# Kernel tuning notes

Hardware: AMD Instinct MI355X
Metric: run time of the kernel (lower is better)

The kernel has to match this reference:

```python
import jax, jax.numpy as jnp
import numpy as np

N, DIM, H, HD, RD, QLR, OLR, G = 64, 4096, 32, 192, 64, 1536, 512, 8
BS, MAXB, L, NBLK, TOPK, EPS = 64, 64, 4096, 4096, 1024, 1e-6
SLOTS = NBLK * BS
SCALE = HD ** -0.5
NEG = -1e30


def _rms(x, w, eps=EPS):
    return x * jax.lax.rsqrt(jnp.mean(x * x, -1, keepdims=True) + eps) * w


def _rope(x, pos):
    # x: [..., RD]; pos broadcastable to x.shape[:-1]; interleaved pairs
    half = RD // 2
    inv = 1.0 / (10000.0 ** (jnp.arange(half, dtype=jnp.float32) * 2.0 / RD))
    ang = pos[..., None].astype(jnp.float32) * inv  # [..., half]
    c, s = jnp.cos(ang), jnp.sin(ang)
    xr = x.reshape(x.shape[:-1] + (half, 2))
    x0, x1 = xr[..., 0], xr[..., 1]
    return jnp.stack([x0 * c - x1 * s, x0 * s + x1 * c], -1).reshape(x.shape)


def setup_inputs() -> dict:
    key = jax.random.key(0)
    ks = jax.random.split(key, 12)
    block_tables = jax.random.permutation(ks[0], jnp.arange(N * MAXB, dtype=jnp.int32)).reshape(N, MAXB)
    context_lens = jax.random.randint(ks[1], (N,), 1, L, dtype=jnp.int32)
    last = context_lens - 1
    slot_mapping = (block_tables[jnp.arange(N), last // BS] * BS + last % BS).astype(jnp.int32)
    def w(k, shape, fan_in):
        return jax.random.normal(k, shape, jnp.float32) * (fan_in ** -0.5)
    return {
        'x': jax.random.normal(ks[2], (N, DIM), jnp.float32),
        'kv_cache': jax.random.normal(ks[3], (SLOTS, HD), jnp.float32),
        'block_tables': block_tables,
        'context_lens': context_lens,
        'slot_mapping': slot_mapping,
        'wq_a_w': w(ks[4], (QLR, DIM), DIM),
        'q_norm_w': jnp.ones((QLR,), jnp.float32),
        'wq_b_w': w(ks[5], (H * HD, QLR), QLR),
        'wkv_w': w(ks[6], (HD, DIM), DIM),
        'kv_norm_w': jnp.ones((HD,), jnp.float32),
        'wo_a_w': w(ks[7], (G, OLR, H * HD // G), H * HD // G),
        'wo_b_w': w(ks[8], (DIM, G * OLR), G * OLR),
        'attn_sink': jax.random.normal(ks[9], (H,), jnp.float32),
    }


def reference(x, kv_cache, block_tables, context_lens, slot_mapping,
              wq_a_w, q_norm_w, wq_b_w, wkv_w, kv_norm_w,
              wo_a_w, wo_b_w, attn_sink):
    pos = (context_lens - 1).astype(jnp.float32)  # [N] query positions
    # --- queries: LoRA down-proj -> RMSNorm -> up-proj -> heads ---
    q = _rms(x @ wq_a_w.T, q_norm_w) @ wq_b_w.T            # [N, H*HD]
    q = q.reshape(N, H, HD)
    q = jnp.concatenate([q[..., :HD - RD], _rope(q[..., HD - RD:], pos[:, None])], -1)
    # --- new KV latent + paged write (slot_mapping scatter) ---
    kv = _rms(x @ wkv_w.T, kv_norm_w)                       # [N, HD]
    kv = jnp.concatenate([kv[:, :HD - RD], _rope(kv[:, HD - RD:], pos)], -1)
    cache = kv_cache.at[slot_mapping].set(kv)
    # --- paged gather into dense per-request view [N, L, HD] ---
    ar = jnp.arange(L)
    slot = block_tables[:, ar // BS] * BS + ar % BS         # [N, L]
    valid = ar[None, :] < context_lens[:, None]             # [N, L]
    kv_dense = cache[jnp.where(valid, slot, 0)]
    kv_dense = jnp.where(valid[..., None], kv_dense, 0.0)
    # --- sparse top-k attention with sink logit ---
    logits = jnp.einsum('nhd,nld->nhl', q, kv_dense) * SCALE
    logits = jnp.where(valid[:, None, :], logits, NEG)
    vals, idx = jax.lax.top_k(logits, TOPK)                 # [N, H, K]
    sink = attn_sink[None, :, None]                         # [1, H, 1]
    m = jnp.maximum(jnp.max(vals, -1, keepdims=True), sink)
    e = jnp.exp(vals - m)
    denom = jnp.sum(e, -1, keepdims=True) + jnp.exp(sink - m)
    p = e / denom                                           # [N, H, K]
    probs = jnp.put_along_axis(jnp.zeros_like(logits), idx, p, axis=-1, inplace=False)
    o = jnp.einsum('nhl,nld->nhd', probs, kv_dense)         # [N, H, HD]
    # --- grouped LoRA output projection ---
    og = o.reshape(N, G, H * HD // G)
    lat = jnp.einsum('ngi,goi->ngo', og, wo_a_w).reshape(N, G * OLR)
    return lat @ wo_b_w.T                                   # [N, DIM]
```

## Files before the change

kernel.cpp:

```cpp
#include <hip/hip_runtime.h>
#include <hip/hip_bf16.h>

static constexpr float EPS_   = 1e-6f;
static constexpr float SCALE_ = 0.07216878364870323f;
static constexpr float LOG2_1E4_OVER_32 = 13.287712379549449f / 32.0f;

static constexpr long OFF_QLAT = 0;
static constexpr long OFF_Q    = OFF_QLAT + 64L * 1536;
static constexpr long OFF_KVR  = OFF_Q    + 64L * 6144;
static constexpr long OFF_O    = OFF_KVR  + 64L * 192;
static constexpr long OFF_LAT  = OFF_O    + 64L * 6144;
static constexpr long ZERO_F   = OFF_LAT  + 64L * 4096;
static constexpr long OFF_SELM = ZERO_F;
static constexpr long OFF_SELI = OFF_SELM + 2048;
static constexpr long OFF_SELT = OFF_SELI + 2048;
static constexpr long OFF_LOG  = OFF_SELT + 2048;

typedef __attribute__((ext_vector_type(8))) short bf16x8;
typedef __attribute__((ext_vector_type(4))) float f32x4;

__device__ __forceinline__ unsigned fkey(float f) {
    unsigned u = __float_as_uint(f);
    return (u & 0x80000000u) ? ~u : (u | 0x80000000u);
}
__device__ __forceinline__ float kval(unsigned k) {
    unsigned u = (k & 0x80000000u) ? (k ^ 0x80000000u) : ~k;
    return __uint_as_float(u);
}
__device__ __forceinline__ unsigned short f2bf(float f) {
    __hip_bfloat16 h = __float2bfloat16(f);
    return *reinterpret_cast<unsigned short*>(&h);
}
__device__ __forceinline__ bf16x8 pack8(float4 v0, float4 v1) {
    bf16x8 s;
    s[0] = (short)f2bf(v0.x); s[1] = (short)f2bf(v0.y);
    s[2] = (short)f2bf(v0.z); s[3] = (short)f2bf(v0.w);
    s[4] = (short)f2bf(v1.x); s[5] = (short)f2bf(v1.y);
    s[6] = (short)f2bf(v1.z); s[7] = (short)f2bf(v1.w);
    return s;
}

__device__ __forceinline__ void hist_add_agg(int* hist, unsigned bin, bool pred) {
    const int lane = (int)(threadIdx.x & 63);
    while (__any(pred)) {
        unsigned long long act = __ballot(pred);
        int leader = __ffsll((unsigned long long)act) - 1;
        unsigned lbin = (unsigned)__shfl((int)bin, leader, 64);
        bool mine = pred && (bin == lbin);
        unsigned long long grp = __ballot(mine);
        if (lane == leader) atomicAdd(&hist[lbin], (int)__popcll(grp));
        if (mine) pred = false;
    }
}

template <int TN>
__global__ __launch_bounds__(256) void gemm_mfma(
    const float* __restrict__ Xb, const float* __restrict__ Wb,
    float* __restrict__ Cb, int K, int ldX, int ldC, int kslice,
    long sXz, long sWz, long sCz)
{
    const float* X = Xb + (long)blockIdx.z * sXz;
    const float* W = Wb + (long)blockIdx.z * sWz;
    float*       C = Cb + (long)blockIdx.z * sCz;
    const int col0 = blockIdx.x * TN;
    const int k0   = blockIdx.y * kslice;

    __shared__ unsigned short Xs[64 * 64];
    __shared__ unsigned short Ws[TN * 64];

    const int t = threadIdx.x;
    const int w = t >> 6, lane = t & 63;
    const int m16 = lane & 15, qd = lane >> 4;
    constexpr int NT = TN / 64;

    f32x4 acc[4][NT];
#pragma unroll
    for (int mt = 0; mt < 4; ++mt)
#pragma unroll
        for (int nt = 0; nt < NT; ++nt) acc[mt][nt] = (f32x4){0.f, 0.f, 0.f, 0.f};

    for (int kt = k0; kt < k0 + kslice; kt += 64) {
#pragma unroll
        for (int i = 0; i < 2; ++i) {
            int idx = t + i * 256;
            int r = idx >> 3, u = idx & 7;
            const float* p = X + (long)r * ldX + kt + u * 8;
            float4 v0 = *(const float4*)p, v1 = *(const float4*)(p + 4);
            *(bf16x8*)(Xs + r * 64 + (u ^ (r & 7)) * 8) = pack8(v0, v1);
        }
#pragma unroll
        for (int i = 0; i < TN / 32; ++i) {
            int idx = t + i * 256;
            int r = idx >> 3, u = idx & 7;
            const float* p = W + (long)(col0 + r) * K + kt + u * 8;
            float4 v0 = *(const float4*)p, v1 = *(const float4*)(p + 4);
            *(bf16x8*)(Ws + r * 64 + (u ^ (r & 7)) * 8) = pack8(v0, v1);
        }
        __syncthreads();
#pragma unroll
        for (int ks = 0; ks < 2; ++ks) {
            int u = ks * 4 + qd;
            bf16x8 a[4], b[NT];
#pragma unroll
            for (int mt = 0; mt < 4; ++mt) {
                int row = mt * 16 + m16;
                a[mt] = *(const bf16x8*)(Xs + row * 64 + (u ^ (row & 7)) * 8);
            }
#pragma unroll
            for (int nt = 0; nt < NT; ++nt) {
                int row = (w * NT + nt) * 16 + m16;
                b[nt] = *(const bf16x8*)(Ws + row * 64 + (u ^ (row & 7)) * 8);
            }
#pragma unroll
            for (int mt = 0; mt < 4; ++mt)
#pragma unroll
                for (int nt = 0; nt < NT; ++nt)
                    acc[mt][nt] = __builtin_amdgcn_mfma_f32_16x16x32_bf16(a[mt], b[nt], acc[mt][nt], 0, 0, 0);
        }
        __syncthreads();
    }
#pragma unroll
    for (int mt = 0; mt < 4; ++mt)
#pragma unroll
        for (int nt = 0; nt < NT; ++nt) {
            int col = col0 + (w * NT + nt) * 16 + m16;
#pragma unroll
            for (int r = 0; r < 4; ++r) {
                int row = mt * 16 + qd * 4 + r;
                atomicAdd(&C[(long)row * ldC + col], acc[mt][nt][r]);
            }
        }
}

__global__ __launch_bounds__(256) void rms_rows(
    float* __restrict__ x, const float* __restrict__ w, int len)
{
    __shared__ float fred[4];
    float* row = x + (long)blockIdx.x * len;
    int t = threadIdx.x;
    float ss = 0.f;
    for (int l = t; l < len; l += 256) { float v = row[l]; ss += v * v; }
#pragma unroll
    for (int off = 32; off; off >>= 1) ss += __shfl_xor(ss, off, 64);
    if ((t & 63) == 0) fred[t >> 6] = ss;
    __syncthreads();
    ss = fred[0] + fred[1] + fred[2] + fred[3];
    float scale = rsqrtf(ss / (float)len + EPS_);
    for (int l = t; l < len; l += 256) row[l] = row[l] * scale * w[l];
}

__global__ __launch_bounds__(256) void rope_q(float* __restrict__ q,
                                              const int* __restrict__ cl)
{
    int n = blockIdx.x;
    float pos = (float)(cl[n] - 1);
    int t = threadIdx.x;
#pragma unroll
    for (int i = 0; i < 4; ++i) {
        int f = t + i * 256;
        int h = f >> 5, r = f & 31;
        float inv = exp2f(-(float)r * LOG2_1E4_OVER_32);
        float ang = pos * inv;
        float sn, cs;
        sincosf(ang, &sn, &cs);
        float* p = q + (long)n * 6144 + h * 192 + 128 + 2 * r;
        float x0 = p[0], x1 = p[1];
        p[0] = x0 * cs - x1 * sn;
        p[1] = x0 * sn + x1 * cs;
    }
}

__global__ __launch_bounds__(256) void kv_post(
    const float* __restrict__ kvr, const float* __restrict__ wnorm,
    const int* __restrict__ cl, const int* __restrict__ smap,
    float* __restrict__ kvcache)
{
    __shared__ float s[192];
    __shared__ float fred[4];
    int n = blockIdx.x, t = threadIdx.x;
    float v = (t < 192) ? kvr[(long)n * 192 + t] : 0.f;
    float ss = v * v;
#pragma unroll
    for (int off = 32; off; off >>= 1) ss += __shfl_xor(ss, off, 64);
    if ((t & 63) == 0) fred[t >> 6] = ss;
    __syncthreads();
    ss = fred[0] + fred[1] + fred[2] + fred[3];
    float scale = rsqrtf(ss / 192.f + EPS_);
    if (t < 192) s[t] = v * scale * wnorm[t];
    __syncthreads();
    if (t < 32) {
        float pos = (float)(cl[n] - 1);
        float inv = exp2f(-(float)t * LOG2_1E4_OVER_32);
        float ang = pos * inv;
        float sn, cs;
        sincosf(ang, &sn, &cs);
        float x0 = s[128 + 2 * t], x1 = s[128 + 2 * t + 1];
        s[128 + 2 * t]     = x0 * cs - x1 * sn;
        s[128 + 2 * t + 1] = x0 * sn + x1 * cs;
    }
    __syncthreads();
    if (t < 192) kvcache[(long)smap[n] * 192 + t] = s[t];
}

__global__ __launch_bounds__(256) void attn_logits_mfma(
    const float* __restrict__ q, const float* __restrict__ kvc,
    const int* __restrict__ bt, const int* __restrict__ cl,
    float* __restrict__ logits)
{
    const int n = blockIdx.y, sbase = blockIdx.x * 256;
    const int ctx = cl[n];
    if (sbase >= ctx) return;

    __shared__ unsigned short qs[32 * 192];
    __shared__ unsigned short kvs[128 * 192];
    const int t = threadIdx.x;
    const int w = t >> 6, lane = t & 63;
    const int m16 = lane & 15, qd = lane >> 4;

#pragma unroll
    for (int i = 0; i < 3; ++i) {
        int idx = t + i * 256;
        int h = idx / 24, u = idx - h * 24;
        const float* p = q + (long)n * 6144 + h * 192 + u * 8;
        float4 v0 = *(const float4*)p, v1 = *(const float4*)(p + 4);
        *(bf16x8*)(qs + h * 192 + (u ^ (h & 7)) * 8) = pack8(v0, v1);
    }

    for (int c = 0; c < 2; ++c) {
        const int base = sbase + c * 128;
        if (base >= ctx) break;

#pragma unroll
        for (int i = 0; i < 12; ++i) {
            int idx = t + i * 256;
            int l = idx / 24, u = idx - l * 24;
            int gl = min(base + l, ctx - 1);
            int slot = bt[n * 64 + (gl >> 6)] * 64 + (gl & 63);
            const float* p = kvc + (long)slot * 192 + u * 8;
            float4 v0 = *(const float4*)p, v1 = *(const float4*)(p + 4);
            *(bf16x8*)(kvs + l * 192 + (u ^ (l & 7)) * 8) = pack8(v0, v1);
        }
        __syncthreads();

        f32x4 acc[2][2];
#pragma unroll
        for (int mt = 0; mt < 2; ++mt)
#pragma unroll
            for (int nt = 0; nt < 2; ++nt) acc[mt][nt] = (f32x4){0.f, 0.f, 0.f, 0.f};

#pragma unroll
        for (int ks = 0; ks < 6; ++ks) {
            int u = ks * 4 + qd;
            bf16x8 a[2], b[2];
#pragma unroll
            for (int mt = 0; mt < 2; ++mt) {
                int row = mt * 16 + m16;
                a[mt] = *(const bf16x8*)(qs + row * 192 + (u ^ (row & 7)) * 8);
            }
#pragma unroll
            for (int nt = 0; nt < 2; ++nt) {
                int row = (2 * w + nt) * 16 + m16;
                b[nt] = *(const bf16x8*)(kvs + row * 192 + (u ^ (row & 7)) * 8);
            }
#pragma unroll
            for (int mt = 0; mt < 2; ++mt)
#pragma unroll
                for (int nt = 0; nt < 2; ++nt)
                    acc[mt][nt] = __builtin_amdgcn_mfma_f32_16x16x32_bf16(a[mt], b[nt], acc[mt][nt], 0, 0, 0);
        }
#pragma unroll
        for (int mt = 0; mt < 2; ++mt)
#pragma unroll
            for (int nt = 0; nt < 2; ++nt) {
                int l = base + (2 * w + nt) * 16 + m16;
#pragma unroll
                for (int r = 0; r < 4; ++r) {
                    int h = mt * 16 + qd * 4 + r;
                    logits[((long)(n * 32 + h) << 12) + l] = acc[mt][nt][r] * SCALE_;
                }
            }
        __syncthreads();
    }
}

__global__ __launch_bounds__(256) void select_topk(
    const float* __restrict__ logits, const int* __restrict__ cl,
    const float* __restrict__ sink, float* __restrict__ selm,
    float* __restrict__ seli, unsigned* __restrict__ selt)
{
    int nh = blockIdx.x, n = nh >> 5, h = nh & 31;
    int ctx = cl[n];
    const float* row = logits + ((long)nh << 12);

    __shared__ unsigned keys[4096];
    __shared__ int hist[256];
    __shared__ float fred[4];
    __shared__ int wsumi[4];
    __shared__ unsigned s_pref;
    __shared__ int s_R;

    int t = threadIdx.x;
    int lane = t & 63, wv = t >> 6;
    bool need_radix = (ctx > 1024);

    hist[t] = 0;
    __syncthreads();

    float mx = -3.0e38f;
    for (int l0 = 0; l0 < ctx; l0 += 256) {
        int l = l0 + t;
        bool valid = l < ctx;
        unsigned k = 0;
        if (valid) {
            float v = row[l];
            k = fkey(v);
            keys[l] = k;
            mx = fmaxf(mx, v);
        }
        if (need_radix) hist_add_agg(hist, k >> 24, valid);
    }
#pragma unroll
    for (int off = 32; off; off >>= 1) mx = fmaxf(mx, __shfl_xor(mx, off, 64));
    if (lane == 0) fred[wv] = mx;
    __syncthreads();
    mx = fmaxf(fmaxf(fred[0], fred[1]), fmaxf(fred[2], fred[3]));

    unsigned tau = 0;
    if (need_radix) {
        unsigned pref = 0;
        int R = 1024;
        for (int round = 3; round >= 0; --round) {
            int sh = round * 8;
            if (round < 3) {
                hist[t] = 0;
                __syncthreads();
                for (int l0 = 0; l0 < ctx; l0 += 256) {
                    int l = l0 + t;
                    if (l < ctx) {
                        unsigned k = keys[l];
                        if ((k >> (sh + 8)) == (pref >> (sh + 8)))
                            atomicAdd(&hist[(k >> sh) & 255], 1);
                    }
                }
                __syncthreads();
            }
            int hv = hist[t];
            int v = hv;
#pragma unroll
            for (int off = 1; off < 64; off <<= 1) {
                int u2 = __shfl_down(v, off, 64);
                if (lane + off < 64) v += u2;
            }
            if (lane == 0) wsumi[wv] = v;
            __syncthreads();
            int above = 0;
#pragma unroll
            for (int w2 = 1; w2 < 4; ++w2)
                if (wv + w2 < 4) above += wsumi[wv + w2];
            int cum = (v - hv) + above;
            if (cum < R && cum + hv >= R) {
                s_pref = pref | ((unsigned)t << sh);
                s_R = R - cum;
            }
            __syncthreads();
            pref = s_pref;
            R = s_R;
            __syncthreads();
        }
        tau = pref;
    }

    float m = fmaxf(mx, sink[h]);
    float part = 0.f;
    for (int l = t; l < ctx; l += 256) {
        unsigned k = keys[l];
        if (k >= tau) part += __expf(kval(k) - m);
    }
#pragma unroll
    for (int off = 32; off; off >>= 1) part += __shfl_xor(part, off, 64);
    __syncthreads();
    if (lane == 0) fred[wv] = part;
    __syncthreads();
    if (t == 0) {
        float denom = fred[0] + fred[1] + fred[2] + fred[3] + __expf(sink[h] - m);
        selm[nh] = m;
        seli[nh] = 1.0f / denom;
        selt[nh] = tau;
    }
}

__global__ __launch_bounds__(256) void attn_wsum_mfma(
    const float* __restrict__ logits, const float* __restrict__ kvc,
    const int* __restrict__ bt, const int* __restrict__ cl,
    const float* __restrict__ selm, const float* __restrict__ seli,
    const unsigned* __restrict__ selt, float* __restrict__ o)
{
    const int n = blockIdx.y, sbase = blockIdx.x * 256;
    const int ctx = cl[n];
    if (sbase >= ctx) return;

    __shared__ unsigned short ps[32 * 128];
    __shared__ unsigned short kvt[192 * 128];
    const int t = threadIdx.x;
    const int w = t >> 6, lane = t & 63;
    const int m16 = lane & 15, qd = lane >> 4;

    float sm[2], sinv[2];
    unsigned stau[2];
#pragma unroll
    for (int i = 0; i < 2; ++i) {
        int nh = n * 32 + ((t + i * 256) >> 4);
        sm[i] = selm[nh];
        sinv[i] = seli[nh];
        stau[i] = selt[nh];
    }

    f32x4 acc[2][3];
#pragma unroll
    for (int mt = 0; mt < 2; ++mt)
#pragma unroll
        for (int nt = 0; nt < 3; ++nt) acc[mt][nt] = (f32x4){0.f, 0.f, 0.f, 0.f};

    for (int c = 0; c < 2; ++c) {
        const int base = sbase + c * 128;
        if (base >= ctx) break;
        const int vcount = min(128, ctx - base);

#pragma unroll
        for (int i = 0; i < 2; ++i) {
            int idx = t + i * 256;
            int hh = idx >> 4, u = idx & 15;
            int nh = n * 32 + hh;
            const float* lp = logits + ((long)nh << 12) + base + u * 8;
            float4 v0 = *(const float4*)lp, v1 = *(const float4*)(lp + 4);
            float vv[8] = {v0.x, v0.y, v0.z, v0.w, v1.x, v1.y, v1.z, v1.w};
            bf16x8 s;
#pragma unroll
            for (int j = 0; j < 8; ++j) {
                int ll = u * 8 + j;
                float p = 0.f;
                if (ll < vcount && fkey(vv[j]) >= stau[i]) p = __expf(vv[j] - sm[i]) * sinv[i];
                s[j] = (short)f2bf(p);
            }
            *(bf16x8*)(ps + hh * 128 + (u ^ (hh & 7)) * 8) = s;
        }
#pragma unroll
        for (int i = 0; i < 24; ++i) {
            int f = t + i * 256;
            int l = f & 127, d4 = f >> 7;
            int gl = min(base + l, ctx - 1);
            int slot = bt[n * 64 + (gl >> 6)] * 64 + (gl & 63);
            float4 v = *(const float4*)(kvc + (long)slot * 192 + d4 * 4);
            float vv[4] = {v.x, v.y, v.z, v.w};
#pragma unroll
            for (int e = 0; e < 4; ++e) {
                int d = d4 * 4 + e;
                int scol = (l & 7) | ((((l >> 3) ^ (d & 7)) & 15) << 3);
                kvt[d * 128 + scol] = f2bf(vv[e]);
            }
        }
        __syncthreads();

#pragma unroll
        for (int ks = 0; ks < 4; ++ks) {
            int u = ks * 4 + qd;
            bf16x8 a[2], b[3];
#pragma unroll
            for (int mt = 0; mt < 2; ++mt) {
                int row = mt * 16 + m16;
                a[mt] = *(const bf16x8*)(ps + row * 128 + (u ^ (row & 7)) * 8);
            }
#pragma unroll
            for (int nt = 0; nt < 3; ++nt) {
                int row = (3 * w + nt) * 16 + m16;
                b[nt] = *(const bf16x8*)(kvt + row * 128 + (u ^ (row & 7)) * 8);
            }
#pragma unroll
            for (int mt = 0; mt < 2; ++mt)
#pragma unroll
                for (int nt = 0; nt < 3; ++nt)
                    acc[mt][nt] = __builtin_amdgcn_mfma_f32_16x16x32_bf16(a[mt], b[nt], acc[mt][nt], 0, 0, 0);
        }
        __syncthreads();
    }

#pragma unroll
    for (int mt = 0; mt < 2; ++mt)
#pragma unroll
        for (int nt = 0; nt < 3; ++nt) {
            int d = (3 * w + nt) * 16 + m16;
#pragma unroll
            for (int r = 0; r < 4; ++r) {
                int h = mt * 16 + qd * 4 + r;
                atomicAdd(&o[(long)n * 6144 + h * 192 + d], acc[mt][nt][r]);
            }
        }
}

extern "C" void kernel_launch(void* const* d_in, const int* in_sizes, int n_in,
                              void* d_out, int out_size, void* d_ws, size_t ws_size,
                              hipStream_t stream)
{
    const float* x    = (const float*)d_in[0];
    float*       kvc  = (float*)d_in[1];
    const int*   bt   = (const int*)d_in[2];
    const int*   cl   = (const int*)d_in[3];
    const int*   smap = (const int*)d_in[4];
    const float* wqa  = (const float*)d_in[5];
    const float* qnw  = (const float*)d_in[6];
    const float* wqb  = (const float*)d_in[7];
    const float* wkv  = (const float*)d_in[8];
    const float* kvnw = (const float*)d_in[9];
    const float* woa  = (const float*)d_in[10];
    const float* wob  = (const float*)d_in[11];
    const float* sink = (const float*)d_in[12];
    float* ws  = (float*)d_ws;
    float* out = (float*)d_out;

    hipMemsetAsync(ws, 0, (size_t)ZERO_F * sizeof(float), stream);
    hipMemsetAsync(out, 0, (size_t)out_size * sizeof(float), stream);

    gemm_mfma<128><<<dim3(12, 16, 1), 256, 0, stream>>>(x, wqa, ws + OFF_QLAT,
                                                        4096, 4096, 1536, 256, 0, 0, 0);
    rms_rows<<<64, 256, 0, stream>>>(ws + OFF_QLAT, qnw, 1536);
    gemm_mfma<128><<<dim3(48, 6, 1), 256, 0, stream>>>(ws + OFF_QLAT, wqb, ws + OFF_Q,
                                                       1536, 1536, 6144, 256, 0, 0, 0);
    rope_q<<<64, 256, 0, stream>>>(ws + OFF_Q, cl);
    gemm_mfma<64><<<dim3(3, 32, 1), 256, 0, stream>>>(x, wkv, ws + OFF_KVR,
                                                      4096, 4096, 192, 128, 0, 0, 0);
    kv_post<<<64, 256, 0, stream>>>(ws + OFF_KVR, kvnw, cl, smap, kvc);
    attn_logits_mfma<<<dim3(16, 64), 256, 0, stream>>>(ws + OFF_Q, kvc, bt, cl,
                                                       ws + OFF_LOG);
    select_topk<<<2048, 256, 0, stream>>>(ws + OFF_LOG, cl, sink,
                                          ws + OFF_SELM, ws + OFF_SELI,
                                          (unsigned*)(ws + OFF_SELT));
    attn_wsum_mfma<<<dim3(16, 64), 256, 0, stream>>>(ws + OFF_LOG, kvc, bt, cl,
                                                     ws + OFF_SELM, ws + OFF_SELI,
                                                     (unsigned*)(ws + OFF_SELT),
                                                     ws + OFF_O);
    gemm_mfma<128><<<dim3(4, 3, 8), 256, 0, stream>>>(ws + OFF_O, woa, ws + OFF_LAT,
                                                      768, 6144, 4096, 256,
                                                      768, 512L * 768, 512);
    gemm_mfma<128><<<dim3(32, 8, 1), 256, 0, stream>>>(ws + OFF_LAT, wob, out,
                                                       4096, 4096, 4096, 512, 0, 0, 0);
}
```

Measured before the change: 549.1 us.

## Fuse q-down and kv projections, merge norms, fold q RoPE into logits

Concatenates the wq_a and wkv weight rows into a single GEMM that writes a combined 1728-wide buffer. It merges the q RMSNorm and the kv norm/RoPE/cache write into one post kernel, and applies q RoPE inside the attention-logits q staging. It also zeroes the output buffer inside the wo_a GEMM in place of a separate memset. This cuts four kernel launches, one memset and a full q read/write pass. In exchange, RoPE is recomputed in every logits block and the GEMM gains a per-row branch when loading weights.

After: 530.2 us. -3.4%, faster.

```diff
diff --git a/kernel.cpp b/kernel.cpp
--- a/kernel.cpp
+++ b/kernel.cpp
@@ -5,10 +5,9 @@
 static constexpr float SCALE_ = 0.07216878364870323f;
 static constexpr float LOG2_1E4_OVER_32 = 13.287712379549449f / 32.0f;
 
-static constexpr long OFF_QLAT = 0;
-static constexpr long OFF_Q    = OFF_QLAT + 64L * 1536;
-static constexpr long OFF_KVR  = OFF_Q    + 64L * 6144;
-static constexpr long OFF_O    = OFF_KVR  + 64L * 192;
+static constexpr long OFF_QK   = 0;
+static constexpr long OFF_Q    = OFF_QK   + 64L * 1728;
+static constexpr long OFF_O    = OFF_Q    + 64L * 6144;
 static constexpr long OFF_LAT  = OFF_O    + 64L * 6144;
 static constexpr long ZERO_F   = OFF_LAT  + 64L * 4096;
 static constexpr long OFF_SELM = ZERO_F;
@@ -57,8 +56,18 @@
 __global__ __launch_bounds__(256) void gemm_mfma(
     const float* __restrict__ Xb, const float* __restrict__ Wb,
     float* __restrict__ Cb, int K, int ldX, int ldC, int kslice,
-    long sXz, long sWz, long sCz)
+    long sXz, long sWz, long sCz,
+    const float* __restrict__ W2, int split,
+    float* __restrict__ zbuf, long zcount)
 {
+    if (zbuf) {
+        int nb = gridDim.x * gridDim.y * gridDim.z;
+        int bid = (blockIdx.z * gridDim.y + blockIdx.y) * gridDim.x + blockIdx.x;
+        long stride = (long)nb * 256;
+        for (long i = (long)bid * 256 + threadIdx.x; i * 4 < zcount; i += stride)
+            *(float4*)(zbuf + i * 4) = (float4){0.f, 0.f, 0.f, 0.f};
+    }
+
     const float* X = Xb + (long)blockIdx.z * sXz;
     const float* W = Wb + (long)blockIdx.z * sWz;
     float*       C = Cb + (long)blockIdx.z * sCz;
@@ -92,7 +101,10 @@
         for (int i = 0; i < TN / 32; ++i) {
             int idx = t + i * 256;
             int r = idx >> 3, u = idx & 7;
-            const float* p = W + (long)(col0 + r) * K + kt + u * 8;
+            int gcol = col0 + r;
+            const float* wrow = (gcol < split) ? (W + (long)gcol * K)
+                                               : (W2 + (long)(gcol - split) * K);
+            const float* p = wrow + kt + u * 8;
             float4 v0 = *(const float4*)p, v1 = *(const float4*)(p + 4);
             *(bf16x8*)(Ws + r * 64 + (u ^ (r & 7)) * 8) = pack8(v0, v1);
         }
@@ -132,61 +144,37 @@
         }
 }
 
-__global__ __launch_bounds__(256) void rms_rows(
-    float* __restrict__ x, const float* __restrict__ w, int len)
+__global__ __launch_bounds__(256) void post_a(
+    float* __restrict__ qk, const float* __restrict__ qnw,
+    const float* __restrict__ kvnw, const int* __restrict__ cl,
+    const int* __restrict__ smap, float* __restrict__ kvcache)
 {
     __shared__ float fred[4];
-    float* row = x + (long)blockIdx.x * len;
-    int t = threadIdx.x;
+    __shared__ float s[192];
+    int n = blockIdx.x, t = threadIdx.x;
+    int lane = t & 63, wv = t >> 6;
+    float* row = qk + (long)n * 1728;
+
     float ss = 0.f;
-    for (int l = t; l < len; l += 256) { float v = row[l]; ss += v * v; }
+    for (int l = t; l < 1536; l += 256) { float v = row[l]; ss += v * v; }
 #pragma unroll
     for (int off = 32; off; off >>= 1) ss += __shfl_xor(ss, off, 64);
-    if ((t & 63) == 0) fred[t >> 6] = ss;
+    if (lane == 0) fred[wv] = ss;
     __syncthreads();
     ss = fred[0] + fred[1] + fred[2] + fred[3];
-    float scale = rsqrtf(ss / (float)len + EPS_);
-    for (int l = t; l < len; l += 256) row[l] = row[l] * scale * w[l];
-}
-
-__global__ __launch_bounds__(256) void rope_q(float* __restrict__ q,
-                                              const int* __restrict__ cl)
-{
-    int n = blockIdx.x;
-    float pos = (float)(cl[n] - 1);
-    int t = threadIdx.x;
-#pragma unroll
-    for (int i = 0; i < 4; ++i) {
-        int f = t + i * 256;
-        int h = f >> 5, r = f & 31;
-        float inv = exp2f(-(float)r * LOG2_1E4_OVER_32);
-        float ang = pos * inv;
-        float sn, cs;
-        sincosf(ang, &sn, &cs);
-        float* p = q + (long)n * 6144 + h * 192 + 128 + 2 * r;
-        float x0 = p[0], x1 = p[1];
-        p[0] = x0 * cs - x1 * sn;
-        p[1] = x0 * sn + x1 * cs;
-    }
-}
-
-__global__ __launch_bounds__(256) void kv_post(
-    const float* __restrict__ kvr, const float* __restrict__ wnorm,
-    const int* __restrict__ cl, const int* __restrict__ smap,
-    float* __restrict__ kvcache)
-{
-    __shared__ float s[192];
-    __shared__ float fred[4];
-    int n = blockIdx.x, t = threadIdx.x;
-    float v = (t < 192) ? kvr[(long)n * 192 + t] : 0.f;
-    float ss = v * v;
-#pragma unroll
-    for (int off = 32; off; off >>= 1) ss += __shfl_xor(ss, off, 64);
-    if ((t & 63) == 0) fred[t >> 6] = ss;
-    __syncthreads();
-    ss = fred[0] + fred[1] + fred[2] + fred[3];
-    float scale = rsqrtf(ss / 192.f + EPS_);
-    if (t < 192) s[t] = v * scale * wnorm[t];
+    float qscale = rsqrtf(ss / 1536.f + EPS_);
+    for (int l = t; l < 1536; l += 256) row[l] = row[l] * qscale * qnw[l];
+
+    float v = (t < 192) ? row[1536 + t] : 0.f;
+    float s2 = v * v;
+#pragma unroll
+    for (int off = 32; off; off >>= 1) s2 += __shfl_xor(s2, off, 64);
+    __syncthreads();
+    if (lane == 0) fred[wv] = s2;
+    __syncthreads();
+    s2 = fred[0] + fred[1] + fred[2] + fred[3];
+    float kscale = rsqrtf(s2 / 192.f + EPS_);
+    if (t < 192) s[t] = v * kscale * kvnw[t];
     __syncthreads();
     if (t < 32) {
         float pos = (float)(cl[n] - 1);
@@ -210,6 +198,7 @@
     const int n = blockIdx.y, sbase = blockIdx.x * 256;
     const int ctx = cl[n];
     if (sbase >= ctx) return;
+    const float pos = (float)(ctx - 1);
 
     __shared__ unsigned short qs[32 * 192];
     __shared__ unsigned short kvs[128 * 192];
@@ -223,6 +212,18 @@
         int h = idx / 24, u = idx - h * 24;
         const float* p = q + (long)n * 6144 + h * 192 + u * 8;
         float4 v0 = *(const float4*)p, v1 = *(const float4*)(p + 4);
+        if (u >= 16) {
+            int r0 = 4 * (u - 16);
+            float sn, cs, a0, a1;
+            sincosf(pos * exp2f(-(float)(r0)     * LOG2_1E4_OVER_32), &sn, &cs);
+            a0 = v0.x * cs - v0.y * sn; a1 = v0.x * sn + v0.y * cs; v0.x = a0; v0.y = a1;
+            sincosf(pos * exp2f(-(float)(r0 + 1) * LOG2_1E4_OVER_32), &sn, &cs);
+            a0 = v0.z * cs - v0.w * sn; a1 = v0.z * sn + v0.w * cs; v0.z = a0; v0.w = a1;
+            sincosf(pos * exp2f(-(float)(r0 + 2) * LOG2_1E4_OVER_32), &sn, &cs);
+            a0 = v1.x * cs - v1.y * sn; a1 = v1.x * sn + v1.y * cs; v1.x = a0; v1.y = a1;
+            sincosf(pos * exp2f(-(float)(r0 + 3) * LOG2_1E4_OVER_32), &sn, &cs);
+            a0 = v1.z * cs - v1.w * sn; a1 = v1.z * sn + v1.w * cs; v1.z = a0; v1.w = a1;
+        }
         *(bf16x8*)(qs + h * 192 + (u ^ (h & 7)) * 8) = pack8(v0, v1);
     }
 
@@ -517,18 +518,17 @@
     float* ws  = (float*)d_ws;
     float* out = (float*)d_out;
 
+    const int BIG = 1 << 30;
+
     hipMemsetAsync(ws, 0, (size_t)ZERO_F * sizeof(float), stream);
-    hipMemsetAsync(out, 0, (size_t)out_size * sizeof(float), stream);
-
-    gemm_mfma<128><<<dim3(12, 16, 1), 256, 0, stream>>>(x, wqa, ws + OFF_QLAT,
-                                                        4096, 4096, 1536, 256, 0, 0, 0);
-    rms_rows<<<64, 256, 0, stream>>>(ws + OFF_QLAT, qnw, 1536);
-    gemm_mfma<128><<<dim3(48, 6, 1), 256, 0, stream>>>(ws + OFF_QLAT, wqb, ws + OFF_Q,
-                                                       1536, 1536, 6144, 256, 0, 0, 0);
-    rope_q<<<64, 256, 0, stream>>>(ws + OFF_Q, cl);
-    gemm_mfma<64><<<dim3(3, 32, 1), 256, 0, stream>>>(x, wkv, ws + OFF_KVR,
-                                                      4096, 4096, 192, 128, 0, 0, 0);
-    kv_post<<<64, 256, 0, stream>>>(ws + OFF_KVR, kvnw, cl, smap, kvc);
+
+    gemm_mfma<64><<<dim3(27, 16, 1), 256, 0, stream>>>(
+        x, wqa, ws + OFF_QK, 4096, 4096, 1728, 256, 0, 0, 0,
+        wkv, 1536, nullptr, 0);
+    post_a<<<64, 256, 0, stream>>>(ws + OFF_QK, qnw, kvnw, cl, smap, kvc);
+    gemm_mfma<128><<<dim3(48, 6, 1), 256, 0, stream>>>(
+        ws + OFF_QK, wqb, ws + OFF_Q, 1536, 1728, 6144, 256, 0, 0, 0,
+        nullptr, BIG, nullptr, 0);
     attn_logits_mfma<<<dim3(16, 64), 256, 0, stream>>>(ws + OFF_Q, kvc, bt, cl,
                                                        ws + OFF_LOG);
     select_topk<<<2048, 256, 0, stream>>>(ws + OFF_LOG, cl, sink,
@@ -538,9 +538,10 @@
                                                      ws + OFF_SELM, ws + OFF_SELI,
                                                      (unsigned*)(ws + OFF_SELT),
                                                      ws + OFF_O);
-    gemm_mfma<128><<<dim3(4, 3, 8), 256, 0, stream>>>(ws + OFF_O, woa, ws + OFF_LAT,
-                                                      768, 6144, 4096, 256,
-                                                      768, 512L * 768, 512);
-    gemm_mfma<128><<<dim3(32, 8, 1), 256, 0, stream>>>(ws + OFF_LAT, wob, out,
-                                                       4096, 4096, 4096, 512, 0, 0, 0);
-}
+    gemm_mfma<128><<<dim3(4, 3, 8), 256, 0, stream>>>(
+        ws + OFF_O, woa, ws + OFF_LAT, 768, 6144, 4096, 256,
+        768, 512L * 768, 512, nullptr, BIG, out, 64L * 4096);
+    gemm_mfma<128><<<dim3(32, 8, 1), 256, 0, stream>>>(
+        ws + OFF_LAT, wob, out, 4096, 4096, 4096, 512, 0, 0, 0,
+        nullptr, BIG, nullptr, 0);
+}
```
